# Kernel optimization log

Hardware: AMD Instinct MI355X
Metric: run time of the kernel (lower is better)

Reference implementation:

```python
import jax, jax.numpy as jnp
import numpy as np

B, T, C = 4, 2048, 2048
H, N = 32, 64          # num_heads, head_size
EPS = 1e-5 * 8.0 ** 2  # GroupNorm eps = 1e-5 * head_size_divisor**2


def setup_inputs() -> dict:
    key = jax.random.key(0)
    ks = jax.random.split(key, 20)
    f = lambda i, shape, s=0.02: jax.random.normal(ks[i], shape, jnp.float32) * s
    return {
        'hidden': jax.random.normal(ks[0], (B, T, C), jnp.float32),
        'time_maa_x': f(1, (C,)), 'time_maa_w': f(2, (C,)), 'time_maa_k': f(3, (C,)),
        'time_maa_v': f(4, (C,)), 'time_maa_r': f(5, (C,)), 'time_maa_g': f(6, (C,)),
        'time_maa_w1': f(7, (C, 160)), 'time_maa_w2': f(8, (5, 32, C)),
        'time_decay': f(9, (C,), 0.5), 'time_decay_w1': f(10, (C, 64)),
        'time_decay_w2': f(11, (64, C)),
        'time_faaaa': f(12, (H, N), 0.5),
        'w_r': f(13, (C, C)), 'w_k': f(14, (C, C)), 'w_v': f(15, (C, C)),
        'w_g': f(16, (C, C)), 'w_o': f(17, (C, C)),
        'ln_w': jnp.ones((C,), jnp.float32), 'ln_b': jnp.zeros((C,), jnp.float32),
    }


def reference(hidden, time_maa_x, time_maa_w, time_maa_k, time_maa_v, time_maa_r,
              time_maa_g, time_maa_w1, time_maa_w2, time_decay, time_decay_w1,
              time_decay_w2, time_faaaa, w_r, w_k, w_v, w_g, w_o, ln_w, ln_b):
    x = hidden
    # time_shift: prepend zero row, drop last (state=None path)
    shifted = jnp.pad(x, ((0, 0), (1, 0), (0, 0)))[:, :-1]
    xx = shifted - x
    # data-dependent low-rank token-shift interpolation (5 lerp channels)
    xm = x + xx * time_maa_x
    t5 = jnp.tanh(jnp.einsum('btc,ce->bte', xm, time_maa_w1)).reshape(B, T, 5, 32)
    m = jnp.einsum('btfe,fec->fbtc', t5, time_maa_w2)  # [5,B,T,C]
    mw, mk, mv, mr, mg = m[0], m[1], m[2], m[3], m[4]
    xd = x + xx * (time_maa_w + mw)
    xk = x + xx * (time_maa_k + mk)
    xv = x + xx * (time_maa_v + mv)
    xr = x + xx * (time_maa_r + mr)
    xg = x + xx * (time_maa_g + mg)
    r = xr @ w_r.T
    k = xk @ w_k.T
    v = xv @ w_v.T
    g = jax.nn.silu(xg @ w_g.T)
    td = time_decay + jnp.tanh(xd @ time_decay_w1) @ time_decay_w2  # [B,T,C]
    w = jnp.exp(-jnp.exp(td))  # per-channel decay in (0,1)
    # [B,T,C] -> [T,B,H,N] for the scan
    to_tbhn = lambda a: a.reshape(B, T, H, N).transpose(1, 0, 2, 3)
    rT, kT, vT, wT = to_tbhn(r), to_tbhn(k), to_tbhn(v), to_tbhn(w)
    u = time_faaaa  # [H,N]
    state0 = jnp.zeros((B, H, N, N), jnp.float32)  # [B,H,key,value]

    def step(state, ins):
        r_t, k_t, v_t, w_t = ins  # each [B,H,N]
        att = k_t[..., :, None] * v_t[..., None, :]        # outer product k v^T
        out_t = jnp.einsum('bhn,bhnm->bhm', r_t,
                           u[None, :, :, None] * att + state)
        new_state = att + w_t[..., None] * state           # decay along key dim
        return new_state, out_t

    _, outs = jax.lax.scan(step, state0, (rT, kT, vT, wT))  # outs [T,B,H,N]
    out = outs.transpose(1, 0, 2, 3)                         # [B,T,H,N]
    # GroupNorm with H groups over C channels, applied per (b,t) sample
    mu = out.mean(-1, keepdims=True)
    var = out.var(-1, keepdims=True)
    out = (out - mu) / jnp.sqrt(var + EPS)
    out = (out * ln_w.reshape(H, N) + ln_b.reshape(H, N)).reshape(B, T, C)
    out = out * g
    return out @ w_o.T
```

## Files before the change

### kernel.cpp

```cpp
#include <hip/hip_runtime.h>
#include <hip/hip_bf16.h>
#include <math.h>

typedef __hip_bfloat16 bf16;
typedef __attribute__((ext_vector_type(8))) short short8;
typedef __attribute__((ext_vector_type(4))) float f32x4;

#define Bb 4
#define Tt 2048
#define Cc 2048
#define Hh 32
#define Nn 64
#define BT (Bb*Tt)
#define Gg 16
#define Ll 128
#define SPLITK 8

__device__ __forceinline__ float b2f(bf16 x) { return __bfloat162float(x); }
__device__ __forceinline__ bf16  f2b(float x) { return __float2bfloat16(x); }

__global__ __launch_bounds__(256) void cvt_kernel(
    const float* __restrict__ in, bf16* __restrict__ out)
{
  int i = blockIdx.x * 256 + threadIdx.x;
  out[i] = f2b(in[i]);
}

__global__ __launch_bounds__(256) void cvt_t2_kernel(
    const float* __restrict__ in, bf16* __restrict__ hi, bf16* __restrict__ lo,
    int N)
{
  int idx = blockIdx.x * 256 + threadIdx.x;
  int n = idx >> 11, k = idx & 2047;
  float v = in[(size_t)k * N + n];
  bf16 h = f2b(v);
  hi[idx] = h;
  lo[idx] = f2b(v - b2f(h));
}

__global__ __launch_bounds__(256) void cvt_w2t_kernel(
    const float* __restrict__ in, bf16* __restrict__ hi, bf16* __restrict__ lo)
{
  int idx = blockIdx.x * 256 + threadIdx.x;
  int c = idx / 160, e = idx - c * 160;
  float v = in[(size_t)e * Cc + c];
  bf16 h = f2b(v);
  hi[idx] = h;
  lo[idx] = f2b(v - b2f(h));
}

__global__ __launch_bounds__(256) void prep_xm_kernel(
    const float* __restrict__ x, const float* __restrict__ maa_x,
    bf16* __restrict__ xm)
{
  int idx = blockIdx.x * 256 + threadIdx.x;
  int c  = idx & (Cc - 1);
  int bt = idx >> 11;
  int t  = bt & (Tt - 1);
  float xv   = x[idx];
  float prev = (t == 0) ? 0.f : x[idx - Cc];
  xm[idx] = f2b(xv + (prev - xv) * maa_x[c]);
}

#define LDA 40

__global__ __launch_bounds__(256) void mfma_gemm_kernel(
    const bf16* __restrict__ A, const bf16* __restrict__ B,
    bf16* __restrict__ outB, float* __restrict__ outF, int mode)
{
  __shared__ bf16 As[128 * LDA];
  __shared__ bf16 Bs[128 * LDA];
  int tid  = threadIdx.x;
  int lane = tid & 63, wid = tid >> 6;
  int wm = wid & 1, wn = wid >> 1;
  int quad = lane >> 4, l16 = lane & 15;
  size_t rowBase = (size_t)blockIdx.x * 128;
  size_t colBase = (size_t)blockIdx.y * 128;

  f32x4 acc[4][4];
  #pragma unroll
  for (int i = 0; i < 4; ++i)
    #pragma unroll
    for (int j = 0; j < 4; ++j)
      acc[i][j] = (f32x4){0.f, 0.f, 0.f, 0.f};

  for (int k0 = 0; k0 < 2048; k0 += 32) {
    #pragma unroll
    for (int pass = 0; pass < 2; ++pass) {
      int chunk = tid + pass * 256;
      int row = chunk >> 2, kc = (chunk & 3) * 8;
      short8 av = *(const short8*)(A + (rowBase + row) * 2048 + k0 + kc);
      short8 bv = *(const short8*)(B + (colBase + row) * 2048 + k0 + kc);
      *(short8*)(As + row * LDA + kc) = av;
      *(short8*)(Bs + row * LDA + kc) = bv;
    }
    __syncthreads();
    short8 af[4], bf[4];
    #pragma unroll
    for (int i = 0; i < 4; ++i) {
      af[i] = *(const short8*)(As + (wm * 64 + i * 16 + l16) * LDA + quad * 8);
      bf[i] = *(const short8*)(Bs + (wn * 64 + i * 16 + l16) * LDA + quad * 8);
    }
    #pragma unroll
    for (int i = 0; i < 4; ++i)
      #pragma unroll
      for (int j = 0; j < 4; ++j)
        acc[i][j] = __builtin_amdgcn_mfma_f32_16x16x32_bf16(af[i], bf[j], acc[i][j], 0, 0, 0);
    __syncthreads();
  }

  #pragma unroll
  for (int i = 0; i < 4; ++i) {
    #pragma unroll
    for (int j = 0; j < 4; ++j) {
      int gc = colBase + wn * 64 + j * 16 + l16;
      #pragma unroll
      for (int reg = 0; reg < 4; ++reg) {
        int gr = rowBase + wm * 64 + i * 16 + quad * 4 + reg;
        float v = acc[i][j][reg];
        size_t idx = (size_t)gr * 2048 + gc;
        if (mode == 0)      outB[idx] = f2b(v);
        else if (mode == 2) outB[idx] = f2b(v / (1.f + expf(-v)));
        else                outF[idx] = v;
      }
    }
  }
}

template<int NF>
__global__ __launch_bounds__(256) void mfma_skinny_kernel(
    const bf16* __restrict__ A, const bf16* __restrict__ Bt_hi,
    const bf16* __restrict__ Bt_lo,
    float* __restrict__ partial, int kseg_len)
{
  constexpr int N = NF * 16;
  __shared__ bf16 As[64 * LDA];
  __shared__ bf16 Bs[2 * N * LDA];
  int tid = threadIdx.x;
  int lane = tid & 63, w = tid >> 6;
  int quad = lane >> 4, l16 = lane & 15;
  int rowBase = blockIdx.x * 64;
  int kbeg = blockIdx.y * kseg_len;

  f32x4 acc[NF];
  #pragma unroll
  for (int f = 0; f < NF; ++f) acc[f] = (f32x4){0.f, 0.f, 0.f, 0.f};

  for (int k0 = kbeg; k0 < kbeg + kseg_len; k0 += 32) {
    {
      int row = tid >> 2, kc = (tid & 3) * 8;
      *(short8*)(As + row * LDA + kc) =
          *(const short8*)(A + (size_t)(rowBase + row) * 2048 + k0 + kc);
    }
    for (int c = tid; c < N * 8; c += 256) {
      int half = c >= N * 4;
      int cc = c - half * N * 4;
      int row = cc >> 2, kc = (cc & 3) * 8;
      const bf16* src = half ? Bt_lo : Bt_hi;
      *(short8*)(Bs + (half * N + row) * LDA + kc) =
          *(const short8*)(src + (size_t)row * 2048 + k0 + kc);
    }
    __syncthreads();
    short8 af = *(const short8*)(As + (w * 16 + l16) * LDA + quad * 8);
    #pragma unroll
    for (int f = 0; f < NF; ++f) {
      short8 bh = *(const short8*)(Bs + (f * 16 + l16) * LDA + quad * 8);
      short8 bl = *(const short8*)(Bs + ((N + f * 16 + l16)) * LDA + quad * 8);
      acc[f] = __builtin_amdgcn_mfma_f32_16x16x32_bf16(af, bh, acc[f], 0, 0, 0);
      acc[f] = __builtin_amdgcn_mfma_f32_16x16x32_bf16(af, bl, acc[f], 0, 0, 0);
    }
    __syncthreads();
  }

  #pragma unroll
  for (int f = 0; f < NF; ++f) {
    int gc = f * 16 + l16;
    #pragma unroll
    for (int reg = 0; reg < 4; ++reg) {
      int gr = rowBase + w * 16 + quad * 4 + reg;
      partial[((size_t)blockIdx.y * 8192 + gr) * N + gc] = acc[f][reg];
    }
  }
}

__global__ __launch_bounds__(256) void reduce_tanh_kernel(
    const float* __restrict__ partial, bf16* __restrict__ out, int MN)
{
  int idx = blockIdx.x * 256 + threadIdx.x;
  float s = 0.f;
  #pragma unroll
  for (int j = 0; j < SPLITK; ++j) s += partial[(size_t)j * MN + idx];
  out[idx] = f2b(tanhf(s));
}

#define BM 128
#define BN 128
#define BKk 16

__global__ __launch_bounds__(256) void gemm_kernel(
    const bf16* __restrict__ A, const float* __restrict__ Bm,
    bf16* __restrict__ outB,
    const float* __restrict__ bias,
    int M, int N, int K, int transB, int mode)
{
  __shared__ float As[BKk][BM + 1];
  __shared__ float Bs[BKk][BN + 1];
  int tid = threadIdx.x;
  int rowBase = blockIdx.x * BM;
  int colBase = blockIdx.y * BN;
  int tx = tid & 15, ty = tid >> 4;
  float acc[8][8];
  #pragma unroll
  for (int i = 0; i < 8; ++i)
    #pragma unroll
    for (int j = 0; j < 8; ++j) acc[i][j] = 0.f;

  for (int k0 = 0; k0 < K; k0 += BKk) {
    #pragma unroll
    for (int i = 0; i < 8; ++i) {
      int lin = tid + i * 256;
      int r = lin >> 4, kk = lin & 15;
      int gr = rowBase + r, gk = k0 + kk;
      float val = 0.f;
      if (gr < M && gk < K) val = b2f(A[(size_t)gr * K + gk]);
      As[kk][r] = val;
    }
    #pragma unroll
    for (int i = 0; i < 8; ++i) {
      int lin = tid + i * 256;
      float val = 0.f;
      if (transB) {
        int n = lin >> 4, kk = lin & 15;
        int gn = colBase + n, gk = k0 + kk;
        if (gn < N && gk < K) val = Bm[(size_t)gn * K + gk];
        Bs[kk][n] = val;
      } else {
        int kk = lin >> 7, n = lin & 127;
        int gn = colBase + n, gk = k0 + kk;
        if (gn < N && gk < K) val = Bm[(size_t)gk * N + gn];
        Bs[kk][n] = val;
      }
    }
    __syncthreads();
    #pragma unroll
    for (int kk = 0; kk < BKk; ++kk) {
      float a[8], b[8];
      #pragma unroll
      for (int i = 0; i < 8; ++i) a[i] = As[kk][ty * 8 + i];
      #pragma unroll
      for (int j = 0; j < 8; ++j) b[j] = Bs[kk][tx * 8 + j];
      #pragma unroll
      for (int i = 0; i < 8; ++i)
        #pragma unroll
        for (int j = 0; j < 8; ++j)
          acc[i][j] = fmaf(a[i], b[j], acc[i][j]);
    }
    __syncthreads();
  }
  #pragma unroll
  for (int i = 0; i < 8; ++i) {
    int gr = rowBase + ty * 8 + i;
    if (gr >= M) continue;
    #pragma unroll
    for (int j = 0; j < 8; ++j) {
      int gn = colBase + tx * 8 + j;
      if (gn >= N) continue;
      float v = acc[i][j];
      size_t idx = (size_t)gr * N + gn;
      if (mode == 1)      outB[idx] = f2b(tanhf(v));
      else                outB[idx] = f2b(bias[gn] + v);
    }
  }
}

__global__ __launch_bounds__(256) void lerp5_mfma_kernel(
    const float* __restrict__ x, const bf16* __restrict__ t5,
    const bf16* __restrict__ w2t_hi, const bf16* __restrict__ w2t_lo,
    const float* __restrict__ maa_w, const float* __restrict__ maa_k,
    const float* __restrict__ maa_v, const float* __restrict__ maa_r,
    const float* __restrict__ maa_g,
    bf16* __restrict__ xd, bf16* __restrict__ xk, bf16* __restrict__ xv_,
    bf16* __restrict__ xr, bf16* __restrict__ xg)
{
  int tid  = threadIdx.x;
  int lane = tid & 63, wid = tid >> 6;
  int wm = wid & 1, wn = wid >> 1;
  int quad = lane >> 4, l16 = lane & 15;
  int rowBase = blockIdx.x * 128;
  int colBase = blockIdx.y * 128;

  const float* maas[5] = {maa_w, maa_k, maa_v, maa_r, maa_g};
  bf16* outs[5] = {xd, xk, xv_, xr, xg};

  #pragma unroll
  for (int f = 0; f < 5; ++f) {
    short8 af[4];
    #pragma unroll
    for (int i = 0; i < 4; ++i)
      af[i] = *(const short8*)(t5 +
          (size_t)(rowBase + wm * 64 + i * 16 + l16) * 160 + f * 32 + quad * 8);

    f32x4 acc[4][4];
    #pragma unroll
    for (int i = 0; i < 4; ++i)
      #pragma unroll
      for (int j = 0; j < 4; ++j)
        acc[i][j] = (f32x4){0.f, 0.f, 0.f, 0.f};

    #pragma unroll
    for (int j = 0; j < 4; ++j) {
      size_t boff = (size_t)(colBase + wn * 64 + j * 16 + l16) * 160 + f * 32 + quad * 8;
      short8 bh = *(const short8*)(w2t_hi + boff);
      short8 bl = *(const short8*)(w2t_lo + boff);
      #pragma unroll
      for (int i = 0; i < 4; ++i) {
        acc[i][j] = __builtin_amdgcn_mfma_f32_16x16x32_bf16(af[i], bh, acc[i][j], 0, 0, 0);
        acc[i][j] = __builtin_amdgcn_mfma_f32_16x16x32_bf16(af[i], bl, acc[i][j], 0, 0, 0);
      }
    }

    const float* maa = maas[f];
    bf16* outp = outs[f];
    #pragma unroll
    for (int j = 0; j < 4; ++j) {
      int gc = colBase + wn * 64 + j * 16 + l16;
      float mv = maa[gc];
      #pragma unroll
      for (int i = 0; i < 4; ++i) {
        #pragma unroll
        for (int reg = 0; reg < 4; ++reg) {
          int gr = rowBase + wm * 64 + i * 16 + quad * 4 + reg;
          size_t idx = (size_t)gr * Cc + gc;
          float xv0  = x[idx];
          float prev = ((gr & (Tt - 1)) == 0) ? 0.f : x[idx - Cc];
          outp[idx] = f2b(xv0 + (prev - xv0) * (mv + acc[i][j][reg]));
        }
      }
    }
  }
}

__global__ __launch_bounds__(64) void wkv_local_kernel(
    const bf16* __restrict__ k, const bf16* __restrict__ v,
    const bf16* __restrict__ td,
    float* __restrict__ S_local, float* __restrict__ wp)
{
  int bh = blockIdx.x >> 4;
  int c  = blockIdx.x & 15;
  int b  = bh >> 5, h = bh & 31;
  int j  = threadIdx.x;
  int cn = j >> 4, mg = j & 15;
  __shared__ __align__(16) float kb[2][64];
  __shared__ __align__(16) float wb[2][64];
  __shared__ __align__(16) float vb[2][64];
  f32x4 s[16];
  float wpr[16];
  #pragma unroll
  for (int i = 0; i < 16; ++i) { s[i] = (f32x4){0.f,0.f,0.f,0.f}; wpr[i] = 1.f; }

  size_t base = (size_t)b * Tt * Cc + (size_t)(c * Ll) * Cc + (size_t)h * 64;
  float kv_ = b2f(k[base + j]);
  float wv_ = expf(-expf(b2f(td[base + j])));
  float vv_ = b2f(v[base + j]);
  for (int t = 0; t < Ll; ++t, base += Cc) {
    int p = t & 1;
    kb[p][j] = kv_; wb[p][j] = wv_; vb[p][j] = vv_;
    size_t nb = base + ((t + 1 < Ll) ? Cc : 0);
    kv_ = b2f(k[nb + j]);
    wv_ = expf(-expf(b2f(td[nb + j])));
    vv_ = b2f(v[nb + j]);
    asm volatile("s_waitcnt lgkmcnt(0)" ::: "memory");
    f32x4 vm = *(const f32x4*)(&vb[p][mg * 4]);
    #pragma unroll
    for (int i4 = 0; i4 < 4; ++i4) {
      f32x4 k4 = *(const f32x4*)(&kb[p][cn * 16 + i4 * 4]);
      f32x4 w4 = *(const f32x4*)(&wb[p][cn * 16 + i4 * 4]);
      #pragma unroll
      for (int q = 0; q < 4; ++q) {
        int i = i4 * 4 + q;
        float kn = k4[q], wn = w4[q];
        s[i].x = fmaf(wn, s[i].x, kn * vm.x);
        s[i].y = fmaf(wn, s[i].y, kn * vm.y);
        s[i].z = fmaf(wn, s[i].z, kn * vm.z);
        s[i].w = fmaf(wn, s[i].w, kn * vm.w);
        wpr[i] *= wn;
      }
    }
  }
  #pragma unroll
  for (int i = 0; i < 16; ++i)
    *(f32x4*)(&S_local[((size_t)blockIdx.x * 64 + cn * 16 + i) * 64 + mg * 4]) = s[i];
  if (mg == 0) {
    #pragma unroll
    for (int i = 0; i < 16; ++i)
      wp[blockIdx.x * 64 + cn * 16 + i] = wpr[i];
  }
}

__global__ __launch_bounds__(256) void wkv_combine_kernel(
    const float* __restrict__ S_local, const float* __restrict__ wp,
    float* __restrict__ S_start)
{
  int idx = blockIdx.x * 256 + threadIdx.x;
  int m = idx & 63;
  int n = (idx >> 6) & 63;
  int bh = idx >> 12;
  float cur = 0.f;
  #pragma unroll
  for (int c = 0; c < Gg; ++c) {
    size_t sbase = (((size_t)(bh * Gg + c)) * 64 + n) * 64 + m;
    S_start[sbase] = cur;
    cur = fmaf(wp[(bh * Gg + c) * 64 + n], cur, S_local[sbase]);
  }
}

__global__ __launch_bounds__(64) void wkv_out_kernel(
    const bf16* __restrict__ r, const bf16* __restrict__ k,
    const bf16* __restrict__ v, const bf16* __restrict__ td,
    const float* __restrict__ u, const float* __restrict__ S_start,
    bf16* __restrict__ out)
{
  int bh = blockIdx.x >> 4;
  int c  = blockIdx.x & 15;
  int b  = bh >> 5, h = bh & 31;
  int j  = threadIdx.x;
  int cn = j >> 4, mg = j & 15;
  __shared__ __align__(16) float rb[2][64];
  __shared__ __align__(16) float kb[2][64];
  __shared__ __align__(16) float wb[2][64];
  __shared__ __align__(16) float vb[2][64];
  __shared__ __align__(16) float red[256];
  f32x4 s[16];
  float ur[16];
  #pragma unroll
  for (int i = 0; i < 16; ++i) {
    s[i]  = *(const f32x4*)(&S_start[((size_t)blockIdx.x * 64 + cn * 16 + i) * 64 + mg * 4]);
    ur[i] = u[h * 64 + cn * 16 + i];
  }

  size_t base = (size_t)b * Tt * Cc + (size_t)(c * Ll) * Cc + (size_t)h * 64;
  float rv_ = b2f(r[base + j]);
  float kv_ = b2f(k[base + j]);
  float wv_ = expf(-expf(b2f(td[base + j])));
  float vv_ = b2f(v[base + j]);
  for (int t = 0; t < Ll; ++t, base += Cc) {
    int p = t & 1;
    rb[p][j] = rv_; kb[p][j] = kv_; wb[p][j] = wv_; vb[p][j] = vv_;
    size_t nb = base + ((t + 1 < Ll) ? Cc : 0);
    rv_ = b2f(r[nb + j]);
    kv_ = b2f(k[nb + j]);
    wv_ = expf(-expf(b2f(td[nb + j])));
    vv_ = b2f(v[nb + j]);
    asm volatile("s_waitcnt lgkmcnt(0)" ::: "memory");
    f32x4 vm = *(const f32x4*)(&vb[p][mg * 4]);
    f32x4 acc = (f32x4){0.f, 0.f, 0.f, 0.f};
    #pragma unroll
    for (int i4 = 0; i4 < 4; ++i4) {
      f32x4 r4 = *(const f32x4*)(&rb[p][cn * 16 + i4 * 4]);
      f32x4 k4 = *(const f32x4*)(&kb[p][cn * 16 + i4 * 4]);
      f32x4 w4 = *(const f32x4*)(&wb[p][cn * 16 + i4 * 4]);
      #pragma unroll
      for (int q = 0; q < 4; ++q) {
        int i = i4 * 4 + q;
        float rn = r4[q], kn = k4[q], wn = w4[q], un = ur[i];
        float kvx = kn * vm.x, kvy = kn * vm.y, kvz = kn * vm.z, kvw = kn * vm.w;
        acc.x = fmaf(rn, fmaf(un, kvx, s[i].x), acc.x);
        acc.y = fmaf(rn, fmaf(un, kvy, s[i].y), acc.y);
        acc.z = fmaf(rn, fmaf(un, kvz, s[i].z), acc.z);
        acc.w = fmaf(rn, fmaf(un, kvw, s[i].w), acc.w);
        s[i].x = fmaf(wn, s[i].x, kvx);
        s[i].y = fmaf(wn, s[i].y, kvy);
        s[i].z = fmaf(wn, s[i].z, kvz);
        s[i].w = fmaf(wn, s[i].w, kvw);
      }
    }
    *(f32x4*)(&red[4 * j]) = acc;
    asm volatile("s_waitcnt lgkmcnt(0)" ::: "memory");
    float o = red[j] + red[64 + j] + red[128 + j] + red[192 + j];
    out[base + j] = f2b(o);
  }
}

__global__ __launch_bounds__(256) void gn_gate_kernel(
    const bf16* __restrict__ wkv, const bf16* __restrict__ g,
    const float* __restrict__ lnw, const float* __restrict__ lnb,
    bf16* __restrict__ out)
{
  int bt = blockIdx.x;
  int wv = threadIdx.x >> 6, lane = threadIdx.x & 63;
  const float EPS = 6.4e-4f;
  for (int h = wv; h < Hh; h += 4) {
    size_t base = (size_t)bt * Cc + h * 64;
    float x = b2f(wkv[base + lane]);
    float s = x, s2 = x * x;
    #pragma unroll
    for (int off = 1; off < 64; off <<= 1) {
      s  += __shfl_xor(s, off);
      s2 += __shfl_xor(s2, off);
    }
    float mean = s * (1.f / 64.f);
    float var  = s2 * (1.f / 64.f) - mean * mean;
    float inv  = rsqrtf(var + EPS);
    float normed = (x - mean) * inv * lnw[h * 64 + lane] + lnb[h * 64 + lane];
    out[base + lane] = f2b(normed * b2f(g[base + lane]));
  }
}

extern "C" void kernel_launch(void* const* d_in, const int* in_sizes, int n_in,
                              void* d_out, int out_size, void* d_ws, size_t ws_size,
                              hipStream_t stream) {
  const float* hidden = (const float*)d_in[0];
  const float* maa_x  = (const float*)d_in[1];
  const float* maa_w  = (const float*)d_in[2];
  const float* maa_k  = (const float*)d_in[3];
  const float* maa_v  = (const float*)d_in[4];
  const float* maa_r  = (const float*)d_in[5];
  const float* maa_g  = (const float*)d_in[6];
  const float* maa_w1 = (const float*)d_in[7];
  const float* maa_w2 = (const float*)d_in[8];
  const float* tdecay = (const float*)d_in[9];
  const float* dw1    = (const float*)d_in[10];
  const float* dw2    = (const float*)d_in[11];
  const float* faaaa  = (const float*)d_in[12];
  const float* w_r    = (const float*)d_in[13];
  const float* w_k    = (const float*)d_in[14];
  const float* w_v    = (const float*)d_in[15];
  const float* w_g    = (const float*)d_in[16];
  const float* w_o    = (const float*)d_in[17];
  const float* lnw    = (const float*)d_in[18];
  const float* lnb    = (const float*)d_in[19];
  float* outF = (float*)d_out;
  bf16* rscratch = (bf16*)d_out;

  char* ws = (char*)d_ws;
  const size_t BUF  = (size_t)BT * Cc * sizeof(bf16);
  const size_t WBUF = (size_t)Cc * Cc * sizeof(bf16);
  const size_t MB = 1024 * 1024;
  bf16* buf0 = (bf16*)(ws + 0 * BUF);
  bf16* buf1 = (bf16*)(ws + 1 * BUF);
  bf16* buf2 = (bf16*)(ws + 2 * BUF);
  bf16* buf3 = (bf16*)(ws + 3 * BUF);
  bf16* buf4 = (bf16*)(ws + 4 * BUF);
  char* small = ws + 5 * BUF;
  bf16* t5buf   = (bf16*)(small + 0);
  bf16* abuf    = (bf16*)(small + 4 * MB);
  bf16* w1t_hi  = (bf16*)(small + 5 * MB);
  bf16* w1t_lo  = (bf16*)(small + 5 * MB + 768 * 1024);
  bf16* dw1t_hi = (bf16*)(small + 6 * MB + 512 * 1024);
  bf16* dw1t_lo = (bf16*)(small + 6 * MB + 768 * 1024);
  char* wbase = small + 8 * MB;
  bf16* wrb = (bf16*)(wbase + 0 * WBUF);
  bf16* wkb = (bf16*)(wbase + 1 * WBUF);
  bf16* wvb = (bf16*)(wbase + 2 * WBUF);
  bf16* wgb = (bf16*)(wbase + 3 * WBUF);
  bf16* wob = (bf16*)(wbase + 4 * WBUF);

  bf16* w2t_hi = (bf16*)((char*)d_out + 48 * MB);
  bf16* w2t_lo = (bf16*)((char*)d_out + 49 * MB);

  float* slbuf = (float*)((char*)d_out + BUF);
  float* ssbuf = (float*)buf0;
  float* wpbuf = (float*)t5buf;
  float* pbuf  = (float*)d_out;

  dim3 blk(256);
  const int CVT_G = Cc * Cc / 256;

  cvt_kernel<<<dim3(CVT_G), blk, 0, stream>>>(w_r, wrb);
  cvt_kernel<<<dim3(CVT_G), blk, 0, stream>>>(w_k, wkb);
  cvt_kernel<<<dim3(CVT_G), blk, 0, stream>>>(w_v, wvb);
  cvt_kernel<<<dim3(CVT_G), blk, 0, stream>>>(w_g, wgb);
  cvt_kernel<<<dim3(CVT_G), blk, 0, stream>>>(w_o, wob);
  cvt_t2_kernel<<<dim3(160 * Cc / 256), blk, 0, stream>>>(maa_w1, w1t_hi, w1t_lo, 160);
  cvt_t2_kernel<<<dim3(64 * Cc / 256), blk, 0, stream>>>(dw1, dw1t_hi, dw1t_lo, 64);
  cvt_w2t_kernel<<<dim3(160 * Cc / 256), blk, 0, stream>>>(maa_w2, w2t_hi, w2t_lo);

  prep_xm_kernel<<<dim3(BT * Cc / 256), blk, 0, stream>>>(hidden, maa_x, buf0);

  mfma_skinny_kernel<10><<<dim3(128, SPLITK), blk, 0, stream>>>(
      buf0, w1t_hi, w1t_lo, pbuf, 2048 / SPLITK);
  reduce_tanh_kernel<<<dim3(BT * 160 / 256), blk, 0, stream>>>(pbuf, t5buf,
                                                               BT * 160);

  lerp5_mfma_kernel<<<dim3(64, 16), blk, 0, stream>>>(hidden, t5buf,
      w2t_hi, w2t_lo, maa_w, maa_k, maa_v, maa_r, maa_g,
      buf1, buf2, buf3, buf4, buf0);

  mfma_skinny_kernel<4><<<dim3(128, SPLITK), blk, 0, stream>>>(
      buf1, dw1t_hi, dw1t_lo, pbuf, 2048 / SPLITK);
  reduce_tanh_kernel<<<dim3(BT * 64 / 256), blk, 0, stream>>>(pbuf, abuf,
                                                              BT * 64);
  gemm_kernel<<<dim3(64, 16), blk, 0, stream>>>(abuf, dw2, buf1, tdecay,
                                                BT, Cc, 64, 0, 3);

  mfma_gemm_kernel<<<dim3(64, 16), blk, 0, stream>>>(buf4, wrb, rscratch, nullptr, 0);
  mfma_gemm_kernel<<<dim3(64, 16), blk, 0, stream>>>(buf2, wkb, buf4, nullptr, 0);
  mfma_gemm_kernel<<<dim3(64, 16), blk, 0, stream>>>(buf3, wvb, buf2, nullptr, 0);
  mfma_gemm_kernel<<<dim3(64, 16), blk, 0, stream>>>(buf0, wgb, buf3, nullptr, 2);

  wkv_local_kernel<<<dim3(Bb * Hh * Gg), dim3(64), 0, stream>>>(
      buf4, buf2, buf1, slbuf, wpbuf);
  wkv_combine_kernel<<<dim3(Bb * Hh * Nn * Nn / 256), blk, 0, stream>>>(
      slbuf, wpbuf, ssbuf);
  wkv_out_kernel<<<dim3(Bb * Hh * Gg), dim3(64), 0, stream>>>(
      rscratch, buf4, buf2, buf1, faaaa, ssbuf, buf1);

  gn_gate_kernel<<<dim3(BT), blk, 0, stream>>>(buf1, buf3, lnw, lnb, buf4);

  mfma_gemm_kernel<<<dim3(64, 16), blk, 0, stream>>>(buf4, wob, nullptr, outF, 4);
}
```

Measured before the change: 1.765 ms.

## Use direct global-to-LDS loads with XOR swizzle in GEMM; reorder mix loop

The main bf16 GEMM now loads A/B tiles straight into shared memory with global_load_lds, replacing the register round trip, and uses a packed 32-wide layout with an XOR swizzle in place of the padded stride to avoid bank conflicts. Separately, the lerp-mix kernel is reordered to loop over column tiles outermost and compute all five channels at once, so x and the shifted x are loaded once per element instead of five times. The mix kernel now reloads t5 fragments inside the loop and holds more accumulators at once, which raises register pressure.

New measurement: 1.574 ms. 10.8% less time.

```diff
diff --git a/kernel.cpp b/kernel.cpp
--- a/kernel.cpp
+++ b/kernel.cpp
@@ -19,6 +19,12 @@
 __device__ __forceinline__ float b2f(bf16 x) { return __bfloat162float(x); }
 __device__ __forceinline__ bf16  f2b(float x) { return __float2bfloat16(x); }
 
+__device__ __forceinline__ void gload16(const bf16* g, bf16* l) {
+  __builtin_amdgcn_global_load_lds(
+      (const __attribute__((address_space(1))) void*)g,
+      (__attribute__((address_space(3))) void*)l, 16, 0, 0);
+}
+
 __global__ __launch_bounds__(256) void cvt_kernel(
     const float* __restrict__ in, bf16* __restrict__ out)
 {
@@ -62,14 +68,12 @@
   xm[idx] = f2b(xv + (prev - xv) * maa_x[c]);
 }
 
-#define LDA 40
-
 __global__ __launch_bounds__(256) void mfma_gemm_kernel(
     const bf16* __restrict__ A, const bf16* __restrict__ B,
     bf16* __restrict__ outB, float* __restrict__ outF, int mode)
 {
-  __shared__ bf16 As[128 * LDA];
-  __shared__ bf16 Bs[128 * LDA];
+  __shared__ __align__(16) bf16 As[128 * 32];
+  __shared__ __align__(16) bf16 Bs[128 * 32];
   int tid  = threadIdx.x;
   int lane = tid & 63, wid = tid >> 6;
   int wm = wid & 1, wn = wid >> 1;
@@ -77,6 +81,14 @@
   size_t rowBase = (size_t)blockIdx.x * 128;
   size_t colBase = (size_t)blockIdx.y * 128;
 
+  int seg0 = wid * 2, seg1 = seg0 + 1;
+  int lrow = lane >> 2;
+  int cb = (((lane & 3) ^ ((lrow >> 1) & 3))) * 8;
+  const bf16* ga0 = A + (rowBase + seg0 * 16 + lrow) * 2048 + cb;
+  const bf16* ga1 = A + (rowBase + seg1 * 16 + lrow) * 2048 + cb;
+  const bf16* gb0 = B + (colBase + seg0 * 16 + lrow) * 2048 + cb;
+  const bf16* gb1 = B + (colBase + seg1 * 16 + lrow) * 2048 + cb;
+
   f32x4 acc[4][4];
   #pragma unroll
   for (int i = 0; i < 4; ++i)
@@ -84,22 +96,18 @@
     for (int j = 0; j < 4; ++j)
       acc[i][j] = (f32x4){0.f, 0.f, 0.f, 0.f};
 
+  int fsw = ((l16 >> 1) & 3) * 8;
   for (int k0 = 0; k0 < 2048; k0 += 32) {
-    #pragma unroll
-    for (int pass = 0; pass < 2; ++pass) {
-      int chunk = tid + pass * 256;
-      int row = chunk >> 2, kc = (chunk & 3) * 8;
-      short8 av = *(const short8*)(A + (rowBase + row) * 2048 + k0 + kc);
-      short8 bv = *(const short8*)(B + (colBase + row) * 2048 + k0 + kc);
-      *(short8*)(As + row * LDA + kc) = av;
-      *(short8*)(Bs + row * LDA + kc) = bv;
-    }
+    gload16(ga0 + k0, As + seg0 * 512);
+    gload16(ga1 + k0, As + seg1 * 512);
+    gload16(gb0 + k0, Bs + seg0 * 512);
+    gload16(gb1 + k0, Bs + seg1 * 512);
     __syncthreads();
     short8 af[4], bf[4];
     #pragma unroll
     for (int i = 0; i < 4; ++i) {
-      af[i] = *(const short8*)(As + (wm * 64 + i * 16 + l16) * LDA + quad * 8);
-      bf[i] = *(const short8*)(Bs + (wn * 64 + i * 16 + l16) * LDA + quad * 8);
+      af[i] = *(const short8*)(As + (wm * 64 + i * 16 + l16) * 32 + ((quad * 8) ^ fsw));
+      bf[i] = *(const short8*)(Bs + (wn * 64 + i * 16 + l16) * 32 + ((quad * 8) ^ fsw));
     }
     #pragma unroll
     for (int i = 0; i < 4; ++i)
@@ -126,6 +134,8 @@
     }
   }
 }
+
+#define LDA 40
 
 template<int NF>
 __global__ __launch_bounds__(256) void mfma_skinny_kernel(
@@ -293,48 +303,45 @@
   bf16* outs[5] = {xd, xk, xv_, xr, xg};
 
   #pragma unroll
-  for (int f = 0; f < 5; ++f) {
-    short8 af[4];
-    #pragma unroll
-    for (int i = 0; i < 4; ++i)
-      af[i] = *(const short8*)(t5 +
-          (size_t)(rowBase + wm * 64 + i * 16 + l16) * 160 + f * 32 + quad * 8);
-
-    f32x4 acc[4][4];
-    #pragma unroll
-    for (int i = 0; i < 4; ++i)
-      #pragma unroll
-      for (int j = 0; j < 4; ++j)
-        acc[i][j] = (f32x4){0.f, 0.f, 0.f, 0.f};
-
-    #pragma unroll
-    for (int j = 0; j < 4; ++j) {
-      size_t boff = (size_t)(colBase + wn * 64 + j * 16 + l16) * 160 + f * 32 + quad * 8;
+  for (int j = 0; j < 4; ++j) {
+    int gc = colBase + wn * 64 + j * 16 + l16;
+    f32x4 accJ[5][4];
+    #pragma unroll
+    for (int f = 0; f < 5; ++f)
+      #pragma unroll
+      for (int i = 0; i < 4; ++i)
+        accJ[f][i] = (f32x4){0.f, 0.f, 0.f, 0.f};
+
+    #pragma unroll
+    for (int f = 0; f < 5; ++f) {
+      size_t boff = (size_t)gc * 160 + f * 32 + quad * 8;
       short8 bh = *(const short8*)(w2t_hi + boff);
       short8 bl = *(const short8*)(w2t_lo + boff);
       #pragma unroll
       for (int i = 0; i < 4; ++i) {
-        acc[i][j] = __builtin_amdgcn_mfma_f32_16x16x32_bf16(af[i], bh, acc[i][j], 0, 0, 0);
-        acc[i][j] = __builtin_amdgcn_mfma_f32_16x16x32_bf16(af[i], bl, acc[i][j], 0, 0, 0);
+        short8 af = *(const short8*)(t5 +
+            (size_t)(rowBase + wm * 64 + i * 16 + l16) * 160 + f * 32 + quad * 8);
+        accJ[f][i] = __builtin_amdgcn_mfma_f32_16x16x32_bf16(af, bh, accJ[f][i], 0, 0, 0);
+        accJ[f][i] = __builtin_amdgcn_mfma_f32_16x16x32_bf16(af, bl, accJ[f][i], 0, 0, 0);
       }
     }
 
-    const float* maa = maas[f];
-    bf16* outp = outs[f];
-    #pragma unroll
-    for (int j = 0; j < 4; ++j) {
-      int gc = colBase + wn * 64 + j * 16 + l16;
-      float mv = maa[gc];
-      #pragma unroll
-      for (int i = 0; i < 4; ++i) {
+    float mv[5];
+    #pragma unroll
+    for (int f = 0; f < 5; ++f) mv[f] = maas[f][gc];
+
+    #pragma unroll
+    for (int i = 0; i < 4; ++i) {
+      #pragma unroll
+      for (int reg = 0; reg < 4; ++reg) {
+        int gr = rowBase + wm * 64 + i * 16 + quad * 4 + reg;
+        size_t idx = (size_t)gr * Cc + gc;
+        float xv0  = x[idx];
+        float prev = ((gr & (Tt - 1)) == 0) ? 0.f : x[idx - Cc];
+        float xx = prev - xv0;
         #pragma unroll
-        for (int reg = 0; reg < 4; ++reg) {
-          int gr = rowBase + wm * 64 + i * 16 + quad * 4 + reg;
-          size_t idx = (size_t)gr * Cc + gc;
-          float xv0  = x[idx];
-          float prev = ((gr & (Tt - 1)) == 0) ? 0.f : x[idx - Cc];
-          outp[idx] = f2b(xv0 + (prev - xv0) * (mv + acc[i][j][reg]));
-        }
+        for (int f = 0; f < 5; ++f)
+          outs[f][idx] = f2b(xv0 + xx * (mv[f] + accJ[f][i][reg]));
       }
     }
   }
```
